# Optimization experiments

Measured on AMD Instinct MI355X. Metric: run time of the kernel, lower is better.

Reference implementation:

```python
import jax, jax.numpy as jnp
import numpy as np

N = 4096          # nodes in DAG
K = 14            # parents per non-root node
C = 1 << K        # CPT configurations per node
N_ROOTS = 64      # nodes with no parents
EPS = 1e-6


def setup_inputs() -> dict:
    key = jax.random.key(0)
    # CPT logits: original init is log(p/(1-p)) with p~U[0.1,0.9] -> roughly N(0,1)-scale
    logits = jax.random.normal(key, (N, C), dtype=jnp.float32)
    # DAG structure: node i >= N_ROOTS has K parents drawn from [0, i) => identity order is topological
    rng = np.random.default_rng(0)
    parents = np.zeros((N, K), dtype=np.int32)
    for i in range(N_ROOTS, N):
        parents[i] = rng.integers(0, i, size=K)
    root_mask = np.arange(N) < N_ROOTS
    # binary configuration matrix, MSB-first, same as _configs_matrix
    ints = np.arange(C)
    configs = ((ints[:, None] >> np.arange(K - 1, -1, -1)) & 1).astype(np.float32)  # [C, K]
    return {
        "logits": logits,
        "configs": jnp.asarray(configs),
        "parents": jnp.asarray(parents),
        "root_mask": jnp.asarray(root_mask),
    }


def reference(logits, configs, parents, root_mask):
    min_val = jnp.log(jnp.float32(EPS))
    max_val = jnp.log(jnp.float32(1.0 - EPS))

    def step(log_marg, xs):
        idx, logit_row, par, is_root = xs
        log_p_cpt = jax.nn.log_sigmoid(logit_row)                    # [C]
        plp = jnp.clip(log_marg[par], min_val, max_val)              # [K] parent log-marginals
        log1m = jnp.log1p(-jnp.minimum(jnp.exp(plp), 1.0 - EPS))     # [K] log(1 - p_parent)
        # sum_k configs*plp + (1-configs)*log1m == configs @ (plp - log1m) + sum(log1m)
        log_prod = configs @ (plp - log1m) + jnp.sum(log1m)          # [C]
        lm_nonroot = jax.nn.logsumexp(log_prod + log_p_cpt)
        lm = jnp.where(is_root, log_p_cpt[0], lm_nonroot)
        return log_marg.at[idx].set(lm), None

    n = logits.shape[0]
    init = jnp.zeros((n,), dtype=jnp.float32)
    xs = (jnp.arange(n), logits, parents, root_mask)
    log_marginals, _ = jax.lax.scan(step, init, xs)
    return jnp.exp(log_marginals)
```

## Files before the change

kernel.cpp:

```cpp
#include <hip/hip_runtime.h>
#include <math.h>
#include <stdint.h>


#define NN     4096
#define KK     14
#define CC     16384
#define NROOTS 64
#define NBLK   256
#define NTHR   1024
#define PT     (CC / NTHR)
#define SENTIN 0x7F7F7F7Fu

#define FOLD2(p, x0, x1) fmaf((p), (x1) - (x0), (x0))
#define FOLD8(pA, pB, pC, s0,s1,s2,s3,s4,s5,s6,s7) \
    FOLD2(pC, FOLD2(pB, FOLD2(pA, s0, s1), FOLD2(pA, s2, s3)), \
              FOLD2(pB, FOLD2(pA, s4, s5), FOLD2(pA, s6, s7)))

__global__ __launch_bounds__(NTHR, 4) void bayes_dag_kernel(
    const float* __restrict__ logits,
    const int*   __restrict__ parents,
    float*       __restrict__ out,
    unsigned*    __restrict__ flagv)
{
    __shared__ float pvals[KK];
    __shared__ int   sSlotLds;
    __shared__ int   sParLds;
    __shared__ float redA[NTHR / 64];
    __shared__ float redB[NTHR / 64];

    const int tid  = threadIdx.x;
    const int lane = tid & 63;
    const int wv   = tid >> 6;
    const float LOG2E = 1.4426950408889634f;

    int node = blockIdx.x;
    if (node < NROOTS) {
        if (tid == 0) {
            float x = logits[(size_t)node * CC];
            float p = __builtin_amdgcn_rcpf(1.f + exp2f(-x * LOG2E));
            __hip_atomic_store(&flagv[node], __float_as_uint(p),
                               __ATOMIC_RELAXED, __HIP_MEMORY_SCOPE_AGENT);
            out[node] = p;
        }
        node += NBLK;
    }

    float xs[PT];
    {
        const float* row = logits + (size_t)node * CC;
        #pragma unroll
        for (int m = 0; m < PT; ++m) xs[m] = row[m * NTHR + tid];
    }
    int pcur = 0;
    if (wv == 0 && lane < KK) pcur = parents[node * KK + lane];

    for (; node < NN; node += NBLK) {
        const int nxt    = node + NBLK;
        const int nclamp = (nxt < NN) ? nxt : node;

        const float* nrow = logits + (size_t)nclamp * CC;
        float xn[PT];
        #pragma unroll
        for (int m = 0; m < PT; ++m) xn[m] = nrow[m * NTHR + tid];

        float sig[PT];
        #pragma unroll
        for (int m = 0; m < PT; ++m)
            sig[m] = __builtin_amdgcn_rcpf(1.f + exp2f(-xs[m] * LOG2E));

        if (wv == 0) {
            unsigned v = SENTIN;
            unsigned long long rdy;
            int guard = 0;
            for (;;) {
                if (lane < KK && v == SENTIN)
                    v = __hip_atomic_load(&flagv[pcur], __ATOMIC_RELAXED,
                                          __HIP_MEMORY_SCOPE_AGENT);
                rdy = __ballot(lane >= KK || v != SENTIN);
                if (__popcll(rdy) >= 63) break;
                if (++guard > (1 << 22)) break;
            }
            unsigned long long miss = (~rdy) & 0x3FFFull;
            int s  = miss ? __builtin_ctzll(miss) : -1;
            int sp = __shfl(pcur, (s < 0) ? 0 : s, 64);
            if (lane == 0) { sSlotLds = s; sParLds = sp; }
            if (lane < KK) {
                float pf = __uint_as_float(v);
                pvals[lane] = fminf(fmaxf(pf, 1e-6f), 1.f - 1e-6f);
            }
            if (lane < KK) pcur = parents[nclamp * KK + lane];
        }
        __syncthreads();

        const int s = sSlotLds;
        float pv[KK];
        #pragma unroll
        for (int k = 0; k < KK; ++k) pv[k] = pvals[k];

        float acc, acc1 = 0.f;
        const bool regPair = (s >= 0 && s < 4);
        switch (s) {
            case 0:
                acc  = FOLD8(pv[3],pv[2],pv[1], sig[0],sig[1],sig[2],sig[3],sig[4],sig[5],sig[6],sig[7]);
                acc1 = FOLD8(pv[3],pv[2],pv[1], sig[8],sig[9],sig[10],sig[11],sig[12],sig[13],sig[14],sig[15]);
                break;
            case 1:
                acc  = FOLD8(pv[3],pv[2],pv[0], sig[0],sig[1],sig[2],sig[3],sig[8],sig[9],sig[10],sig[11]);
                acc1 = FOLD8(pv[3],pv[2],pv[0], sig[4],sig[5],sig[6],sig[7],sig[12],sig[13],sig[14],sig[15]);
                break;
            case 2:
                acc  = FOLD8(pv[3],pv[1],pv[0], sig[0],sig[1],sig[4],sig[5],sig[8],sig[9],sig[12],sig[13]);
                acc1 = FOLD8(pv[3],pv[1],pv[0], sig[2],sig[3],sig[6],sig[7],sig[10],sig[11],sig[14],sig[15]);
                break;
            case 3:
                acc  = FOLD8(pv[2],pv[1],pv[0], sig[0],sig[2],sig[4],sig[6],sig[8],sig[10],sig[12],sig[14]);
                acc1 = FOLD8(pv[2],pv[1],pv[0], sig[1],sig[3],sig[5],sig[7],sig[9],sig[11],sig[13],sig[15]);
                break;
            default:
                acc = FOLD2(pv[0],
                        FOLD8(pv[3],pv[2],pv[1], sig[0],sig[1],sig[2],sig[3],sig[4],sig[5],sig[6],sig[7]),
                        FOLD8(pv[3],pv[2],pv[1], sig[8],sig[9],sig[10],sig[11],sig[12],sig[13],sig[14],sig[15]));
                break;
        }

        const int st = (s >= 8) ? (13 - s) : -1;
        #pragma unroll
        for (int t = 0; t < 6; ++t) {
            if (t == st) continue;
            const float p = pv[13 - t];
            {
                float other = __shfl_xor(acc, 1 << t, 64);
                bool  bit   = (lane >> t) & 1;
                float a = bit ? other : acc;
                float b = bit ? acc : other;
                acc = fmaf(p, b - a, a);
            }
            if (regPair) {
                float other = __shfl_xor(acc1, 1 << t, 64);
                bool  bit   = (lane >> t) & 1;
                float a = bit ? other : acc1;
                float b = bit ? acc1 : other;
                acc1 = fmaf(p, b - a, a);
            }
        }

        if (regPair) {
            if (lane == 0) { redA[wv] = acc; redB[wv] = acc1; }
        } else if (st >= 0) {
            if (lane == 0)         redA[wv] = acc;
            if (lane == (1 << st)) redB[wv] = acc;
        } else {
            if (lane == 0) redA[wv] = acc;
        }
        __syncthreads();

        if (wv == 0) {
            const bool pairAB = (s >= 0) && (s < 4 || s >= 8);
            const int  tw     = (s >= 4 && s < 8) ? (7 - s) : -1;
            float v0 = (lane < NTHR / 64) ? redA[lane] : 0.f;
            float v1 = (pairAB && lane < NTHR / 64) ? redB[lane] : 0.f;
            #pragma unroll
            for (int t = 0; t < 4; ++t) {
                if (t == tw) continue;
                const float p = pv[7 - t];
                {
                    float other = __shfl_xor(v0, 1 << t, 64);
                    bool  bit   = (lane >> t) & 1;
                    float a = bit ? other : v0;
                    float b = bit ? v0 : other;
                    v0 = fmaf(p, b - a, a);
                }
                if (pairAB) {
                    float other = __shfl_xor(v1, 1 << t, 64);
                    bool  bit   = (lane >> t) & 1;
                    float a = bit ? other : v1;
                    float b = bit ? v1 : other;
                    v1 = fmaf(p, b - a, a);
                }
            }
            float res;
            if (s < 0) {
                res = v0;
            } else {
                float x0, x1;
                if (tw >= 0) { x0 = __shfl(v0, 0, 64); x1 = __shfl(v0, 1 << tw, 64); }
                else         { x0 = v0; x1 = v1; }
                const int sp = sParLds;
                unsigned u = __hip_atomic_load(&flagv[sp], __ATOMIC_RELAXED,
                                               __HIP_MEMORY_SCOPE_AGENT);
                int guard = 0;
                while (u == SENTIN && ++guard < (1 << 23))
                    u = __hip_atomic_load(&flagv[sp], __ATOMIC_RELAXED,
                                          __HIP_MEMORY_SCOPE_AGENT);
                float ps = fminf(fmaxf(__uint_as_float(u), 1e-6f), 1.f - 1e-6f);
                res = fmaf(ps, x1 - x0, x0);
            }
            if (lane == 0) {
                __hip_atomic_store(&flagv[node], __float_as_uint(res),
                                   __ATOMIC_RELAXED, __HIP_MEMORY_SCOPE_AGENT);
                out[node] = res;
            }
        }

        #pragma unroll
        for (int m = 0; m < PT; ++m) xs[m] = xn[m];
    }
}

extern "C" void kernel_launch(void* const* d_in, const int* in_sizes, int n_in,
                              void* d_out, int out_size, void* d_ws, size_t ws_size,
                              hipStream_t stream) {
    const float* logits  = (const float*)d_in[0];
    const int*   parents = (const int*)d_in[2];
    float*    out   = (float*)d_out;
    unsigned* flagv = (unsigned*)d_ws;

    hipMemsetAsync(flagv, 0x7F, NN * sizeof(unsigned), stream);

    void* args[] = { (void*)&logits, (void*)&parents, (void*)&out, (void*)&flagv };
    hipLaunchCooperativeKernel((const void*)bayes_dag_kernel,
                               dim3(NBLK), dim3(NTHR), args, 0, stream);
}
```

Measured before the change: 521.0 us.

## Ping-pong parent polling between two wavefronts and pipeline sigmoid ahead

The final reduction and the parent-flag polling for the next node now alternate between wavefronts 0 and 1. While one wave finishes node i, the other waits on node i+NBLK's parents and writes double-buffered pvals and slot values. The sigmoid of the next row is computed at the end of each iteration, and the row after that is prefetched, so the transcendental work is off the critical path. This removes one barrier phase from the serial dependency chain. The cost is extra registers, more complex indexing, and a trailing __syncthreads in every iteration.

```diff
diff --git a/kernel.cpp b/kernel.cpp
--- a/kernel.cpp
+++ b/kernel.cpp
@@ -9,6 +9,7 @@
 #define NROOTS 64
 #define NBLK   256
 #define NTHR   1024
+#define NW     (NTHR / 64)
 #define PT     (CC / NTHR)
 #define SENTIN 0x7F7F7F7Fu
 
@@ -16,6 +17,9 @@
 #define FOLD8(pA, pB, pC, s0,s1,s2,s3,s4,s5,s6,s7) \
     FOLD2(pC, FOLD2(pB, FOLD2(pA, s0, s1), FOLD2(pA, s2, s3)), \
               FOLD2(pB, FOLD2(pA, s4, s5), FOLD2(pA, s6, s7)))
+
+#define LDFLAG(p) __hip_atomic_load(&flagv[(p)], __ATOMIC_RELAXED, \
+                                    __HIP_MEMORY_SCOPE_AGENT)
 
 __global__ __launch_bounds__(NTHR, 4) void bayes_dag_kernel(
     const float* __restrict__ logits,
@@ -23,11 +27,10 @@
     float*       __restrict__ out,
     unsigned*    __restrict__ flagv)
 {
-    __shared__ float pvals[KK];
-    __shared__ int   sSlotLds;
-    __shared__ int   sParLds;
-    __shared__ float redA[NTHR / 64];
-    __shared__ float redB[NTHR / 64];
+    __shared__ float pvals[2][KK];
+    __shared__ int   sSlot[2];
+    __shared__ float redA[NW];
+    __shared__ float redB[NW];
 
     const int tid  = threadIdx.x;
     const int lane = tid & 63;
@@ -46,57 +49,56 @@
         node += NBLK;
     }
 
-    float xs[PT];
+    float sig[PT];
     {
         const float* row = logits + (size_t)node * CC;
-        #pragma unroll
-        for (int m = 0; m < PT; ++m) xs[m] = row[m * NTHR + tid];
-    }
-    int pcur = 0;
-    if (wv == 0 && lane < KK) pcur = parents[node * KK + lane];
-
-    for (; node < NN; node += NBLK) {
-        const int nxt    = node + NBLK;
-        const int nclamp = (nxt < NN) ? nxt : node;
-
-        const float* nrow = logits + (size_t)nclamp * CC;
-        float xn[PT];
-        #pragma unroll
-        for (int m = 0; m < PT; ++m) xn[m] = nrow[m * NTHR + tid];
-
-        float sig[PT];
+        float xt[PT];
+        #pragma unroll
+        for (int m = 0; m < PT; ++m) xt[m] = row[m * NTHR + tid];
         #pragma unroll
         for (int m = 0; m < PT; ++m)
-            sig[m] = __builtin_amdgcn_rcpf(1.f + exp2f(-xs[m] * LOG2E));
-
-        if (wv == 0) {
-            unsigned v = SENTIN;
-            unsigned long long rdy;
-            int guard = 0;
-            for (;;) {
-                if (lane < KK && v == SENTIN)
-                    v = __hip_atomic_load(&flagv[pcur], __ATOMIC_RELAXED,
-                                          __HIP_MEMORY_SCOPE_AGENT);
-                rdy = __ballot(lane >= KK || v != SENTIN);
-                if (__popcll(rdy) >= 63) break;
-                if (++guard > (1 << 22)) break;
-            }
-            unsigned long long miss = (~rdy) & 0x3FFFull;
-            int s  = miss ? __builtin_ctzll(miss) : -1;
-            int sp = __shfl(pcur, (s < 0) ? 0 : s, 64);
-            if (lane == 0) { sSlotLds = s; sParLds = sp; }
-            if (lane < KK) {
-                float pf = __uint_as_float(v);
-                pvals[lane] = fminf(fmaxf(pf, 1e-6f), 1.f - 1e-6f);
-            }
-            if (lane < KK) pcur = parents[nclamp * KK + lane];
-        }
-        __syncthreads();
-
-        const int s = sSlotLds;
+            sig[m] = __builtin_amdgcn_rcpf(1.f + exp2f(-xt[m] * LOG2E));
+    }
+    float xn[PT];
+    {
+        int n1 = node + NBLK; if (n1 >= NN) n1 = node;
+        const float* row = logits + (size_t)n1 * CC;
+        #pragma unroll
+        for (int m = 0; m < PT; ++m) xn[m] = row[m * NTHR + tid];
+    }
+
+    int pcur = 0, myS = -1, mySp = 0;
+    if (wv == 0) {
+        if (lane < KK) pcur = parents[node * KK + lane];
+        unsigned v = SENTIN; unsigned long long rdy; int guard = 0;
+        for (;;) {
+            if (lane < KK && v == SENTIN) v = LDFLAG(pcur);
+            rdy = __ballot(lane >= KK || v != SENTIN);
+            if (__popcll(rdy) >= 63) break;
+            if (++guard > (1 << 22)) break;
+        }
+        unsigned long long miss = (~rdy) & 0x3FFFull;
+        myS  = miss ? __builtin_ctzll(miss) : -1;
+        mySp = __shfl(pcur, (myS < 0) ? 0 : myS, 64);
+        if (lane == 0) sSlot[0] = myS;
+        if (lane < KK) {
+            float pf = __uint_as_float(v);
+            pvals[0][lane] = fminf(fmaxf(pf, 1e-6f), 1.f - 1e-6f);
+        }
+        int pn = node + 2 * NBLK; if (pn >= NN) pn = node;
+        if (lane < KK) pcur = parents[pn * KK + lane];
+    } else if (wv == 1) {
+        int pn = node + NBLK; if (pn >= NN) pn = node;
+        if (lane < KK) pcur = parents[pn * KK + lane];
+    }
+    __syncthreads();
+
+    int rp = 0;
+    for (; node < NN; node += NBLK, rp ^= 1) {
+        const int s = sSlot[rp];
         float pv[KK];
         #pragma unroll
-        for (int k = 0; k < KK; ++k) pv[k] = pvals[k];
+        for (int k = 0; k < KK; ++k) pv[k] = pvals[rp][k];
 
         float acc, acc1 = 0.f;
         const bool regPair = (s >= 0 && s < 4);
@@ -155,11 +157,13 @@
         }
         __syncthreads();
 
-        if (wv == 0) {
+        const int node2 = node + NBLK;
+
+        if (wv == rp) {
             const bool pairAB = (s >= 0) && (s < 4 || s >= 8);
             const int  tw     = (s >= 4 && s < 8) ? (7 - s) : -1;
-            float v0 = (lane < NTHR / 64) ? redA[lane] : 0.f;
-            float v1 = (pairAB && lane < NTHR / 64) ? redB[lane] : 0.f;
+            float v0 = (lane < NW) ? redA[lane] : 0.f;
+            float v1 = (pairAB && lane < NW) ? redB[lane] : 0.f;
             #pragma unroll
             for (int t = 0; t < 4; ++t) {
                 if (t == tw) continue;
@@ -186,13 +190,10 @@
                 float x0, x1;
                 if (tw >= 0) { x0 = __shfl(v0, 0, 64); x1 = __shfl(v0, 1 << tw, 64); }
                 else         { x0 = v0; x1 = v1; }
-                const int sp = sParLds;
-                unsigned u = __hip_atomic_load(&flagv[sp], __ATOMIC_RELAXED,
-                                               __HIP_MEMORY_SCOPE_AGENT);
+                unsigned u = LDFLAG(mySp);
                 int guard = 0;
                 while (u == SENTIN && ++guard < (1 << 23))
-                    u = __hip_atomic_load(&flagv[sp], __ATOMIC_RELAXED,
-                                          __HIP_MEMORY_SCOPE_AGENT);
+                    u = LDFLAG(mySp);
                 float ps = fminf(fmaxf(__uint_as_float(u), 1e-6f), 1.f - 1e-6f);
                 res = fmaf(ps, x1 - x0, x0);
             }
@@ -201,10 +202,36 @@
                                    __ATOMIC_RELAXED, __HIP_MEMORY_SCOPE_AGENT);
                 out[node] = res;
             }
-        }
-
-        #pragma unroll
-        for (int m = 0; m < PT; ++m) xs[m] = xn[m];
+        } else if (wv == (rp ^ 1) && node2 < NN) {
+            unsigned v = SENTIN; unsigned long long rdy; int guard = 0;
+            for (;;) {
+                if (lane < KK && v == SENTIN) v = LDFLAG(pcur);
+                rdy = __ballot(lane >= KK || v != SENTIN);
+                if (__popcll(rdy) >= 63) break;
+                if (++guard > (1 << 22)) break;
+            }
+            unsigned long long miss = (~rdy) & 0x3FFFull;
+            myS  = miss ? __builtin_ctzll(miss) : -1;
+            mySp = __shfl(pcur, (myS < 0) ? 0 : myS, 64);
+            if (lane == 0) sSlot[rp ^ 1] = myS;
+            if (lane < KK) {
+                float pf = __uint_as_float(v);
+                pvals[rp ^ 1][lane] = fminf(fmaxf(pf, 1e-6f), 1.f - 1e-6f);
+            }
+            int pn = node + 3 * NBLK; if (pn >= NN) pn = node;
+            if (lane < KK) pcur = parents[pn * KK + lane];
+        }
+
+        #pragma unroll
+        for (int m = 0; m < PT; ++m)
+            sig[m] = __builtin_amdgcn_rcpf(1.f + exp2f(-xn[m] * LOG2E));
+        {
+            int n2 = node + 2 * NBLK; if (n2 >= NN) n2 = node;
+            const float* row = logits + (size_t)n2 * CC;
+            #pragma unroll
+            for (int m = 0; m < PT; ++m) xn[m] = row[m * NTHR + tid];
+        }
+        __syncthreads();
     }
 }
 
```

Result: no change. 511.4 us (-1.8%).
